# Optimization experiments

Measured on AMD Instinct MI355X. Metric: run time of the kernel, lower is better.

## Reference

```python
import jax, jax.numpy as jnp
import numpy as np

B, C, N, K, D = 4, 64, 40960, 16, 128
EPS = 1e-5  # BatchNorm2d default eps


def _bn_relu(x, g, b, m, v):
    # inference BN over channel axis 1, then ReLU (pt_utils.Conv2d default activation)
    scale = g / jnp.sqrt(v + EPS)
    shift = b - m * scale
    return jax.nn.relu(x * scale[None, :, None, None] + shift[None, :, None, None])


def setup_inputs() -> dict:
    key = jax.random.key(0)
    ks = jax.random.split(key, 16)
    feature = jax.random.normal(ks[0], (B, C, N, 1), jnp.float32)
    neigh_idx = jax.random.randint(ks[1], (B, N, K), 0, N)
    w1 = jax.random.normal(ks[2], (C, C), jnp.float32) * 0.05
    w2 = jax.random.normal(ks[3], (D, C), jnp.float32) * 0.05
    w3 = jax.random.normal(ks[4], (D, C), jnp.float32) * 0.05
    def bn(kg, km, kv, n):
        g = 1.0 + 0.1 * jax.random.normal(kg, (n,), jnp.float32)
        b = 0.1 * jax.random.normal(km, (n,), jnp.float32)
        m = 0.1 * jax.random.normal(kv, (n,), jnp.float32)
        v = jax.random.uniform(jax.random.fold_in(kv, 1), (n,), jnp.float32, 0.5, 1.5)
        return g, b, m, v
    g1, b1, m1, v1 = bn(ks[5], ks[6], ks[7], C)
    g2, b2, m2, v2 = bn(ks[8], ks[9], ks[10], D)
    g3, b3, m3, v3 = bn(ks[11], ks[12], ks[13], D)
    return dict(feature=feature, neigh_idx=neigh_idx,
                w1=w1, g1=g1, b1=b1, m1=m1, v1=v1,
                w2=w2, g2=g2, b2=b2, m2=m2, v2=v2,
                w3=w3, g3=g3, b3=b3, m3=m3, v3=v3)


def reference(feature, neigh_idx, w1, g1, b1, m1, v1, w2, g2, b2, m2, v2,
              w3, g3, b3, m3, v3):
    # gather_neighbour: feature [B,C,N,1], neigh_idx [B,N,K] -> [B,C,N,K]
    f = feature[:, :, :, 0]                                   # [B,C,N]
    f_neigh = jax.vmap(lambda fb, ib: fb[:, ib])(f, neigh_idx)  # [B,C,N,K]
    # mlp1: 1x1 conv + BN + ReLU
    h = jnp.einsum('oc,bcnk->bonk', w1, f_neigh)
    h = _bn_relu(h, g1, b1, m1, v1)
    # sum over neighbors
    h = jnp.sum(h, axis=-1, keepdims=True)                    # [B,C,N,1]
    # mlp2
    h = jnp.einsum('oc,bcnk->bonk', w2, h)
    h = _bn_relu(h, g2, b2, m2, v2)
    # mlp3 on original feature (residual branch)
    s = jnp.einsum('oc,bcnk->bonk', w3, feature)
    s = _bn_relu(s, g3, b3, m3, v3)
    return h + s                                              # [B,D,N,1]
```

## Files before the change

### kernel.cpp

```cpp
#include <hip/hip_runtime.h>

#define EPSV 1e-5f
constexpr int Bb = 4, Cc = 64, Nn = 40960, Kk = 16, Dd = 128;
constexpr int G = 4;
constexpr int TPB = Nn / 16;

typedef float f32x4 __attribute__((ext_vector_type(4)));
typedef __bf16 bf16x8 __attribute__((ext_vector_type(8)));
typedef unsigned short us8 __attribute__((ext_vector_type(8)));
typedef unsigned short us4 __attribute__((ext_vector_type(4)));

__device__ inline unsigned short f2bf(float x) {
    unsigned u = __builtin_bit_cast(unsigned, x);
    u += 0x7FFFu + ((u >> 16) & 1u);
    return (unsigned short)(u >> 16);
}

__global__ __launch_bounds__(256) void prep_weights(
    const float* __restrict__ w1, const float* __restrict__ g1, const float* __restrict__ b1,
    const float* __restrict__ m1, const float* __restrict__ v1,
    const float* __restrict__ w2, const float* __restrict__ g2, const float* __restrict__ b2,
    const float* __restrict__ m2, const float* __restrict__ v2,
    const float* __restrict__ w3, const float* __restrict__ g3, const float* __restrict__ b3,
    const float* __restrict__ m3, const float* __restrict__ v3,
    unsigned short* __restrict__ w1s, unsigned short* __restrict__ w2s, unsigned short* __restrict__ w3s,
    float* __restrict__ sh1, float* __restrict__ sh2, float* __restrict__ sh3) {
    const int e = blockIdx.x * 256 + threadIdx.x;
    if (e < 4096) {
        const int o = e >> 6;
        const float sc = g1[o] * rsqrtf(v1[o] + EPSV);
        w1s[e] = f2bf(w1[e] * sc);
    } else if (e < 12288) {
        const int i = e - 4096, o = i >> 6;
        const float sc = g2[o] * rsqrtf(v2[o] + EPSV);
        w2s[i] = f2bf(w2[i] * sc);
    } else if (e < 20480) {
        const int i = e - 12288, o = i >> 6;
        const float sc = g3[o] * rsqrtf(v3[o] + EPSV);
        w3s[i] = f2bf(w3[i] * sc);
    }
    if (e < 64) sh1[e] = b1[e] - m1[e] * (g1[e] * rsqrtf(v1[e] + EPSV));
    else if (e < 192) { const int d = e - 64;  sh2[d] = b2[d] - m2[d] * (g2[d] * rsqrtf(v2[d] + EPSV)); }
    else if (e < 320) { const int d = e - 192; sh3[d] = b3[d] - m3[d] * (g3[d] * rsqrtf(v3[d] + EPSV)); }
}

__global__ __launch_bounds__(256) void passA(const float* __restrict__ f,
                                             const unsigned short* __restrict__ w1s,
                                             const float* __restrict__ sh1,
                                             unsigned short* __restrict__ G1,
                                             unsigned short* __restrict__ f_t) {
    __shared__ float s[64 * 65];
    __shared__ __attribute__((aligned(16))) unsigned short sg1[64 * 72];

    const int tid = threadIdx.x, w = tid >> 6, lane = tid & 63;
    const int c15 = lane & 15, q = lane >> 4;
    const int b = blockIdx.x / 640;
    const int n0 = (blockIdx.x % 640) * 64;

    const float* src = f + ((size_t)b * Cc + w * 16) * Nn + n0 + lane;
#pragma unroll
    for (int i = 0; i < 16; ++i) s[(w * 16 + i) * 65 + lane] = src[(size_t)i * Nn];

    const int o1 = w * 16 + c15;
    const float sh1v = sh1[o1];
    bf16x8 bw1[2];
#pragma unroll
    for (int ks = 0; ks < 2; ++ks)
        bw1[ks] = __builtin_bit_cast(bf16x8, *(const uint4*)(w1s + o1 * 64 + ks * 32 + q * 8));
    __syncthreads();

#pragma unroll
    for (int mt = 0; mt < 4; ++mt) {
        const int pt = mt * 16 + c15;
        us8 A0, A1;
#pragma unroll
        for (int j = 0; j < 8; ++j) A0[j] = f2bf(s[(q * 8 + j) * 65 + pt]);
#pragma unroll
        for (int j = 0; j < 8; ++j) A1[j] = f2bf(s[(32 + q * 8 + j) * 65 + pt]);

        if (mt == w) {
            unsigned short* dst = f_t + ((size_t)b * Nn + n0 + pt) * 64;
            *(uint4*)(dst + q * 8)      = __builtin_bit_cast(uint4, A0);
            *(uint4*)(dst + 32 + q * 8) = __builtin_bit_cast(uint4, A1);
        }

        f32x4 g = {0.f, 0.f, 0.f, 0.f};
        g = __builtin_amdgcn_mfma_f32_16x16x32_bf16(__builtin_bit_cast(bf16x8, A0), bw1[0], g, 0, 0, 0);
        g = __builtin_amdgcn_mfma_f32_16x16x32_bf16(__builtin_bit_cast(bf16x8, A1), bw1[1], g, 0, 0, 0);
#pragma unroll
        for (int r = 0; r < 4; ++r)
            sg1[(mt * 16 + q * 4 + r) * 72 + o1] = f2bf(fmaxf(g[r] + sh1v, 0.f));
    }
    __syncthreads();

    {
        const int p = tid >> 2, ck = tid & 3;
        const uint4 v0 = *(const uint4*)(sg1 + p * 72 + ck * 16);
        const uint4 v1 = *(const uint4*)(sg1 + p * 72 + ck * 16 + 8);
        unsigned short* dst = G1 + ((size_t)b * Nn + n0 + p) * 64 + ck * 16;
        *(uint4*)dst = v0;
        *(uint4*)(dst + 8) = v1;
    }
}

__global__ __launch_bounds__(256, 4) void passB(
    const unsigned short* __restrict__ G1, const unsigned short* __restrict__ f_t,
    const int* __restrict__ idx,
    const unsigned short* __restrict__ w2s, const unsigned short* __restrict__ w3s,
    const float* __restrict__ sh2, const float* __restrict__ sh3,
    float* __restrict__ out) {
    __shared__ __attribute__((aligned(16))) unsigned short s_h1[16 * 72];
    __shared__ float s_out[32 * 133];

    const int tid  = threadIdx.x;
    const int wave = tid >> 6;
    const int lane = tid & 63;
    const int c15  = lane & 15;
    const int q    = lane >> 4;
    const int pg   = tid >> 4;
    const int cg   = tid & 15;

    const int xcd = blockIdx.x & 7;
    const int jb  = blockIdx.x >> 3;
    const int b   = xcd >> 1;
    const int nb0 = (((xcd & 1) * 320) + jb) * (G * 16);

    float sh2v[2], sh3v[2];
    bf16x8 bw2[2][2], bw3[2][2];
#pragma unroll
    for (int nt = 0; nt < 2; ++nt) {
        const int d = wave * 32 + nt * 16 + c15;
        sh2v[nt] = sh2[d];
        sh3v[nt] = sh3[d];
#pragma unroll
        for (int ks = 0; ks < 2; ++ks) {
            bw2[nt][ks] = __builtin_bit_cast(bf16x8, *(const uint4*)(w2s + d * 64 + ks * 32 + q * 8));
            bw3[nt][ks] = __builtin_bit_cast(bf16x8, *(const uint4*)(w3s + d * 64 + ks * 32 + q * 8));
        }
    }

    const unsigned short* G1b = G1 + (size_t)b * Nn * 64;
    const unsigned short* ftb = f_t + (size_t)b * Nn * 64;
    const int* idxp = idx + ((size_t)b * Nn + nb0) * Kk;

    int myidx = idxp[tid];

    for (int g = 0; g < G; ++g) {
        const int n0 = nb0 + g * 16;

        const int myidxN = (g + 1 < G) ? idxp[(g + 1) * 256 + tid] : 0;

        const unsigned short* ftrow = ftb + (size_t)(n0 + c15) * 64;
        const bf16x8 af0 = __builtin_bit_cast(bf16x8, *(const uint4*)(ftrow + q * 8));
        const bf16x8 af1 = __builtin_bit_cast(bf16x8, *(const uint4*)(ftrow + 32 + q * 8));

        float a0 = 0.f, a1 = 0.f, a2 = 0.f, a3 = 0.f;
#pragma unroll
        for (int k = 0; k < 16; ++k) {
            const int nb = __shfl(myidx, (pg & 3) * 16 + k, 64);
            const uint2 d2 = *(const uint2*)(G1b + (size_t)nb * 64 + cg * 4);
            a0 += __builtin_bit_cast(float, d2.x << 16);
            a1 += __builtin_bit_cast(float, d2.x & 0xffff0000u);
            a2 += __builtin_bit_cast(float, d2.y << 16);
            a3 += __builtin_bit_cast(float, d2.y & 0xffff0000u);
        }
        myidx = myidxN;

        __syncthreads();
        us4 hv;
        hv[0] = f2bf(a0); hv[1] = f2bf(a1); hv[2] = f2bf(a2); hv[3] = f2bf(a3);
        *(us4*)(s_h1 + pg * 72 + cg * 4) = hv;
        __syncthreads();

        const unsigned short* h1row = s_h1 + c15 * 72;
        const bf16x8 ah0 = __builtin_bit_cast(bf16x8, *(const uint4*)(h1row + q * 8));
        const bf16x8 ah1 = __builtin_bit_cast(bf16x8, *(const uint4*)(h1row + 32 + q * 8));

        const int prow = (g & 1) * 16;
#pragma unroll
        for (int nt = 0; nt < 2; ++nt) {
            f32x4 h2 = {sh2v[nt], sh2v[nt], sh2v[nt], sh2v[nt]};
            f32x4 s3 = {sh3v[nt], sh3v[nt], sh3v[nt], sh3v[nt]};
            h2 = __builtin_amdgcn_mfma_f32_16x16x32_bf16(ah0, bw2[nt][0], h2, 0, 0, 0);
            h2 = __builtin_amdgcn_mfma_f32_16x16x32_bf16(ah1, bw2[nt][1], h2, 0, 0, 0);
            s3 = __builtin_amdgcn_mfma_f32_16x16x32_bf16(af0, bw3[nt][0], s3, 0, 0, 0);
            s3 = __builtin_amdgcn_mfma_f32_16x16x32_bf16(af1, bw3[nt][1], s3, 0, 0, 0);
            const int d = wave * 32 + nt * 16 + c15;
#pragma unroll
            for (int r = 0; r < 4; ++r)
                s_out[(prow + q * 4 + r) * 133 + d] = fmaxf(h2[r], 0.f) + fmaxf(s3[r], 0.f);
        }
        __syncthreads();

        if (g & 1) {
            const int np = n0 - 16;
            const int dd = tid >> 3;
            const int ck = tid & 7;
#pragma unroll
            for (int r4 = 0; r4 < 4; ++r4) {
                const int d = r4 * 32 + dd;
                f32x4 v;
#pragma unroll
                for (int i = 0; i < 4; ++i) v[i] = s_out[(ck * 4 + i) * 133 + d];
                __builtin_nontemporal_store(v, (f32x4*)(out + ((size_t)b * Dd + d) * Nn + np + ck * 4));
            }
        }
    }
}

extern "C" void kernel_launch(void* const* d_in, const int* in_sizes, int n_in,
                              void* d_out, int out_size, void* d_ws, size_t ws_size,
                              hipStream_t stream) {
    const float* feature = (const float*)d_in[0];
    const int*   neigh   = (const int*)d_in[1];
    const float* w1 = (const float*)d_in[2];
    const float* g1 = (const float*)d_in[3];
    const float* b1 = (const float*)d_in[4];
    const float* m1 = (const float*)d_in[5];
    const float* v1 = (const float*)d_in[6];
    const float* w2 = (const float*)d_in[7];
    const float* g2 = (const float*)d_in[8];
    const float* b2 = (const float*)d_in[9];
    const float* m2 = (const float*)d_in[10];
    const float* v2 = (const float*)d_in[11];
    const float* w3 = (const float*)d_in[12];
    const float* g3 = (const float*)d_in[13];
    const float* b3 = (const float*)d_in[14];
    const float* m3 = (const float*)d_in[15];
    const float* v3 = (const float*)d_in[16];
    float* out = (float*)d_out;

    const size_t SZ_G1 = (size_t)Bb * Nn * 64 * 2;
    const size_t SZ_FT = (size_t)Bb * Nn * 64 * 2;

    char* ws = (char*)d_ws;
    unsigned short* G1  = (unsigned short*)ws;
    unsigned short* f_t = (unsigned short*)(ws + SZ_G1);
    char* wbase = ws + SZ_G1 + SZ_FT;

    unsigned short* w1s = (unsigned short*)wbase;
    unsigned short* w2s = (unsigned short*)(wbase + 8192);
    unsigned short* w3s = (unsigned short*)(wbase + 24576);
    float* sh1 = (float*)(wbase + 40960);
    float* sh2 = (float*)(wbase + 41216);
    float* sh3 = (float*)(wbase + 41728);

    prep_weights<<<80, 256, 0, stream>>>(w1, g1, b1, m1, v1, w2, g2, b2, m2, v2,
                                         w3, g3, b3, m3, v3, w1s, w2s, w3s, sh1, sh2, sh3);
    passA<<<Bb * 640, 256, 0, stream>>>(feature, w1s, sh1, G1, f_t);
    passB<<<(Bb * TPB) / G, 256, 0, stream>>>(G1, f_t, neigh, w2s, w3s,
                                              sh2, sh3, out);
}
```

Baseline: 209.9 us.

## Fuse weight prep, pass A and pass B into one cooperative persistent kernel

Replaces the three separate launches (weight prep, passA, passB) with one persistent cooperative kernel. Each block folds the BN scales into the weights itself, runs passA tiles in a grid-stride loop, waits at a grid-wide barrier, then runs passB groups with an XCD-aware remapping of work. The aim is to remove launch gaps and the kernel-boundary drain between passes. In exchange it adds a grid sync, redundant per-block weight preparation, and relies on the occupancy check allowing 1024 or more resident blocks.

```diff
diff --git a/kernel.cpp b/kernel.cpp
--- a/kernel.cpp
+++ b/kernel.cpp
@@ -1,9 +1,12 @@
 #include <hip/hip_runtime.h>
+#include <hip/hip_cooperative_groups.h>
 
 #define EPSV 1e-5f
 constexpr int Bb = 4, Cc = 64, Nn = 40960, Kk = 16, Dd = 128;
 constexpr int G = 4;
 constexpr int TPB = Nn / 16;
+constexpr int NTILE_A = Bb * 640;
+constexpr int NGRP_B  = (Bb * TPB) / G;
 
 typedef float f32x4 __attribute__((ext_vector_type(4)));
 typedef __bf16 bf16x8 __attribute__((ext_vector_type(8)));
@@ -14,6 +17,186 @@
     unsigned u = __builtin_bit_cast(unsigned, x);
     u += 0x7FFFu + ((u >> 16) & 1u);
     return (unsigned short)(u >> 16);
+}
+
+__global__ __launch_bounds__(256, 5) void fused(
+    const float* __restrict__ f, const int* __restrict__ idx,
+    const float* __restrict__ w1, const float* __restrict__ g1, const float* __restrict__ b1,
+    const float* __restrict__ m1, const float* __restrict__ v1,
+    const float* __restrict__ w2, const float* __restrict__ g2, const float* __restrict__ b2,
+    const float* __restrict__ m2, const float* __restrict__ v2,
+    const float* __restrict__ w3, const float* __restrict__ g3, const float* __restrict__ b3,
+    const float* __restrict__ m3, const float* __restrict__ v3,
+    unsigned short* __restrict__ G1, unsigned short* __restrict__ f_t,
+    float* __restrict__ out, const int nwg) {
+    __shared__ __attribute__((aligned(16))) char smem[25856];
+    float* s            = (float*)smem;
+    unsigned short* sg1 = (unsigned short*)(smem + 16640);
+    unsigned short* s_h1 = (unsigned short*)smem;
+    float* s_out        = (float*)(smem + 2304);
+
+    const int tid = threadIdx.x, wave = tid >> 6, lane = tid & 63;
+    const int c15 = lane & 15, q = lane >> 4;
+    const int bid = blockIdx.x;
+
+    {
+        const int o1 = wave * 16 + c15;
+        const float sc1 = g1[o1] * rsqrtf(v1[o1] + EPSV);
+        const float sh1v = b1[o1] - m1[o1] * sc1;
+        bf16x8 bw1[2];
+#pragma unroll
+        for (int ks = 0; ks < 2; ++ks) {
+            us8 t;
+#pragma unroll
+            for (int j = 0; j < 8; ++j) t[j] = f2bf(w1[o1 * 64 + ks * 32 + q * 8 + j] * sc1);
+            bw1[ks] = __builtin_bit_cast(bf16x8, t);
+        }
+
+        for (int tt = bid; tt < NTILE_A; tt += nwg) {
+            const int b = tt / 640;
+            const int n0 = (tt - b * 640) * 64;
+
+            const float* src = f + ((size_t)b * Cc + wave * 16) * Nn + n0 + lane;
+#pragma unroll
+            for (int i = 0; i < 16; ++i) s[(wave * 16 + i) * 65 + lane] = src[(size_t)i * Nn];
+            __syncthreads();
+
+#pragma unroll
+            for (int mt = 0; mt < 4; ++mt) {
+                const int pt = mt * 16 + c15;
+                us8 A0, A1;
+#pragma unroll
+                for (int j = 0; j < 8; ++j) A0[j] = f2bf(s[(q * 8 + j) * 65 + pt]);
+#pragma unroll
+                for (int j = 0; j < 8; ++j) A1[j] = f2bf(s[(32 + q * 8 + j) * 65 + pt]);
+
+                if (mt == wave) {
+                    unsigned short* dst = f_t + ((size_t)b * Nn + n0 + pt) * 64;
+                    *(uint4*)(dst + q * 8)      = __builtin_bit_cast(uint4, A0);
+                    *(uint4*)(dst + 32 + q * 8) = __builtin_bit_cast(uint4, A1);
+                }
+
+                f32x4 g = {0.f, 0.f, 0.f, 0.f};
+                g = __builtin_amdgcn_mfma_f32_16x16x32_bf16(__builtin_bit_cast(bf16x8, A0), bw1[0], g, 0, 0, 0);
+                g = __builtin_amdgcn_mfma_f32_16x16x32_bf16(__builtin_bit_cast(bf16x8, A1), bw1[1], g, 0, 0, 0);
+#pragma unroll
+                for (int r = 0; r < 4; ++r)
+                    sg1[(mt * 16 + q * 4 + r) * 72 + (wave * 16 + c15)] = f2bf(fmaxf(g[r] + sh1v, 0.f));
+            }
+            __syncthreads();
+
+            {
+                const int p = tid >> 2, ck = tid & 3;
+                const uint4 v0 = *(const uint4*)(sg1 + p * 72 + ck * 16);
+                const uint4 v1 = *(const uint4*)(sg1 + p * 72 + ck * 16 + 8);
+                unsigned short* dst = G1 + ((size_t)b * Nn + n0 + p) * 64 + ck * 16;
+                *(uint4*)dst = v0;
+                *(uint4*)(dst + 8) = v1;
+            }
+            __syncthreads();
+        }
+    }
+
+    float sh2v[2], sh3v[2];
+    bf16x8 bw2[2][2], bw3[2][2];
+#pragma unroll
+    for (int nt = 0; nt < 2; ++nt) {
+        const int d = wave * 32 + nt * 16 + c15;
+        const float sc2 = g2[d] * rsqrtf(v2[d] + EPSV);
+        const float sc3 = g3[d] * rsqrtf(v3[d] + EPSV);
+        sh2v[nt] = b2[d] - m2[d] * sc2;
+        sh3v[nt] = b3[d] - m3[d] * sc3;
+#pragma unroll
+        for (int ks = 0; ks < 2; ++ks) {
+            us8 t2, t3;
+#pragma unroll
+            for (int j = 0; j < 8; ++j) {
+                t2[j] = f2bf(w2[d * 64 + ks * 32 + q * 8 + j] * sc2);
+                t3[j] = f2bf(w3[d * 64 + ks * 32 + q * 8 + j] * sc3);
+            }
+            bw2[nt][ks] = __builtin_bit_cast(bf16x8, t2);
+            bw3[nt][ks] = __builtin_bit_cast(bf16x8, t3);
+        }
+    }
+
+    cooperative_groups::this_grid().sync();
+
+    const int pg = tid >> 4;
+    const int cg = tid & 15;
+
+    for (int v = bid; v < NGRP_B; v += nwg) {
+        const int xcd = v & 7;
+        const int jb  = v >> 3;
+        const int b   = xcd >> 1;
+        const int nb0 = (((xcd & 1) * 320) + jb) * (G * 16);
+
+        const unsigned short* G1b = G1 + (size_t)b * Nn * 64;
+        const unsigned short* ftb = f_t + (size_t)b * Nn * 64;
+        const int* idxp = idx + ((size_t)b * Nn + nb0) * Kk;
+
+        int myidx = idxp[tid];
+
+        for (int g = 0; g < G; ++g) {
+            const int n0 = nb0 + g * 16;
+            const int myidxN = (g + 1 < G) ? idxp[(g + 1) * 256 + tid] : 0;
+
+            const unsigned short* ftrow = ftb + (size_t)(n0 + c15) * 64;
+            const bf16x8 af0 = __builtin_bit_cast(bf16x8, *(const uint4*)(ftrow + q * 8));
+            const bf16x8 af1 = __builtin_bit_cast(bf16x8, *(const uint4*)(ftrow + 32 + q * 8));
+
+            float a0 = 0.f, a1 = 0.f, a2 = 0.f, a3 = 0.f;
+#pragma unroll
+            for (int k = 0; k < 16; ++k) {
+                const int nb = __shfl(myidx, (pg & 3) * 16 + k, 64);
+                const uint2 d2 = *(const uint2*)(G1b + (size_t)nb * 64 + cg * 4);
+                a0 += __builtin_bit_cast(float, d2.x << 16);
+                a1 += __builtin_bit_cast(float, d2.x & 0xffff0000u);
+                a2 += __builtin_bit_cast(float, d2.y << 16);
+                a3 += __builtin_bit_cast(float, d2.y & 0xffff0000u);
+            }
+            myidx = myidxN;
+
+            __syncthreads();
+            us4 hv;
+            hv[0] = f2bf(a0); hv[1] = f2bf(a1); hv[2] = f2bf(a2); hv[3] = f2bf(a3);
+            *(us4*)(s_h1 + pg * 72 + cg * 4) = hv;
+            __syncthreads();
+
+            const unsigned short* h1row = s_h1 + c15 * 72;
+            const bf16x8 ah0 = __builtin_bit_cast(bf16x8, *(const uint4*)(h1row + q * 8));
+            const bf16x8 ah1 = __builtin_bit_cast(bf16x8, *(const uint4*)(h1row + 32 + q * 8));
+
+            const int prow = (g & 1) * 16;
+#pragma unroll
+            for (int nt = 0; nt < 2; ++nt) {
+                f32x4 h2 = {sh2v[nt], sh2v[nt], sh2v[nt], sh2v[nt]};
+                f32x4 s3 = {sh3v[nt], sh3v[nt], sh3v[nt], sh3v[nt]};
+                h2 = __builtin_amdgcn_mfma_f32_16x16x32_bf16(ah0, bw2[nt][0], h2, 0, 0, 0);
+                h2 = __builtin_amdgcn_mfma_f32_16x16x32_bf16(ah1, bw2[nt][1], h2, 0, 0, 0);
+                s3 = __builtin_amdgcn_mfma_f32_16x16x32_bf16(af0, bw3[nt][0], s3, 0, 0, 0);
+                s3 = __builtin_amdgcn_mfma_f32_16x16x32_bf16(af1, bw3[nt][1], s3, 0, 0, 0);
+                const int d = wave * 32 + nt * 16 + c15;
+#pragma unroll
+                for (int r = 0; r < 4; ++r)
+                    s_out[(prow + q * 4 + r) * 133 + d] = fmaxf(h2[r], 0.f) + fmaxf(s3[r], 0.f);
+            }
+            __syncthreads();
+
+            if (g & 1) {
+                const int np = n0 - 16;
+                const int dd = tid >> 3;
+                const int ck = tid & 7;
+#pragma unroll
+                for (int r4 = 0; r4 < 4; ++r4) {
+                    const int d = r4 * 32 + dd;
+                    f32x4 vv;
+#pragma unroll
+                    for (int i = 0; i < 4; ++i) vv[i] = s_out[(ck * 4 + i) * 133 + d];
+                    __builtin_nontemporal_store(vv, (f32x4*)(out + ((size_t)b * Dd + d) * Nn + np + ck * 4));
+                }
+            }
+        }
+    }
 }
 
 __global__ __launch_bounds__(256) void prep_weights(
@@ -77,13 +260,11 @@
         for (int j = 0; j < 8; ++j) A0[j] = f2bf(s[(q * 8 + j) * 65 + pt]);
 #pragma unroll
         for (int j = 0; j < 8; ++j) A1[j] = f2bf(s[(32 + q * 8 + j) * 65 + pt]);
-
         if (mt == w) {
             unsigned short* dst = f_t + ((size_t)b * Nn + n0 + pt) * 64;
             *(uint4*)(dst + q * 8)      = __builtin_bit_cast(uint4, A0);
             *(uint4*)(dst + 32 + q * 8) = __builtin_bit_cast(uint4, A1);
         }
-
         f32x4 g = {0.f, 0.f, 0.f, 0.f};
         g = __builtin_amdgcn_mfma_f32_16x16x32_bf16(__builtin_bit_cast(bf16x8, A0), bw1[0], g, 0, 0, 0);
         g = __builtin_amdgcn_mfma_f32_16x16x32_bf16(__builtin_bit_cast(bf16x8, A1), bw1[1], g, 0, 0, 0);
@@ -147,7 +328,6 @@
 
     for (int g = 0; g < G; ++g) {
         const int n0 = nb0 + g * 16;
-
         const int myidxN = (g + 1 < G) ? idxp[(g + 1) * 256 + tid] : 0;
 
         const unsigned short* ftrow = ftb + (size_t)(n0 + c15) * 64;
@@ -238,16 +418,44 @@
     unsigned short* f_t = (unsigned short*)(ws + SZ_G1);
     char* wbase = ws + SZ_G1 + SZ_FT;
 
-    unsigned short* w1s = (unsigned short*)wbase;
-    unsigned short* w2s = (unsigned short*)(wbase + 8192);
-    unsigned short* w3s = (unsigned short*)(wbase + 24576);
-    float* sh1 = (float*)(wbase + 40960);
-    float* sh2 = (float*)(wbase + 41216);
-    float* sh3 = (float*)(wbase + 41728);
-
-    prep_weights<<<80, 256, 0, stream>>>(w1, g1, b1, m1, v1, w2, g2, b2, m2, v2,
-                                         w3, g3, b3, m3, v3, w1s, w2s, w3s, sh1, sh2, sh3);
-    passA<<<Bb * 640, 256, 0, stream>>>(feature, w1s, sh1, G1, f_t);
-    passB<<<(Bb * TPB) / G, 256, 0, stream>>>(G1, f_t, neigh, w2s, w3s,
-                                              sh2, sh3, out);
-}
+    static int coop_grid = []() -> int {
+        int dev = 0;
+        if (hipGetDevice(&dev) != hipSuccess) return 0;
+        int attr = 0;
+        if (hipDeviceGetAttribute(&attr, hipDeviceAttributeCooperativeLaunch, dev) != hipSuccess || !attr)
+            return 0;
+        int nb = 0;
+        if (hipOccupancyMaxActiveBlocksPerMultiprocessor(&nb, fused, 256, 0) != hipSuccess)
+            return 0;
+        int ncu = 0;
+        if (hipDeviceGetAttribute(&ncu, hipDeviceAttributeMultiprocessorCount, dev) != hipSuccess)
+            return 0;
+        const long cap = (long)nb * (long)ncu;
+        if (cap >= 1280) return 1280;
+        if (cap >= 1024) return 1024;
+        return 0;
+    }();
+
+    if (coop_grid > 0) {
+        int nwg = coop_grid;
+        void* args[] = {
+            (void*)&feature, (void*)&neigh,
+            (void*)&w1, (void*)&g1, (void*)&b1, (void*)&m1, (void*)&v1,
+            (void*)&w2, (void*)&g2, (void*)&b2, (void*)&m2, (void*)&v2,
+            (void*)&w3, (void*)&g3, (void*)&b3, (void*)&m3, (void*)&v3,
+            (void*)&G1, (void*)&f_t, (void*)&out, (void*)&nwg};
+        (void)hipLaunchCooperativeKernel((const void*)fused, dim3(nwg), dim3(256), args, 0, stream);
+    } else {
+        unsigned short* w1s = (unsigned short*)wbase;
+        unsigned short* w2s = (unsigned short*)(wbase + 8192);
+        unsigned short* w3s = (unsigned short*)(wbase + 24576);
+        float* sh1 = (float*)(wbase + 40960);
+        float* sh2 = (float*)(wbase + 41216);
+        float* sh3 = (float*)(wbase + 41728);
+        prep_weights<<<80, 256, 0, stream>>>(w1, g1, b1, m1, v1, w2, g2, b2, m2, v2,
+                                             w3, g3, b3, m3, v3, w1s, w2s, w3s, sh1, sh2, sh3);
+        passA<<<Bb * 640, 256, 0, stream>>>(feature, w1s, sh1, G1, f_t);
+        passB<<<(Bb * TPB) / G, 256, 0, stream>>>(G1, f_t, neigh, w2s, w3s,
+                                                  sh2, sh3, out);
+    }
+}
```

Result: no change. 210.3 us (+0.2%).

## Restructure passA to skip LDS staging and double-buffer passB h1 tile

Applied to the files above, without the earlier changes.

passA now has each lane load its own point's 64 channels straight from global memory and convert them to bf16 in registers. The float LDS transpose tile and one barrier go away, and the MFMA operands are swapped so the weights act as A and the features as B. passB double-buffers the s_h1 tile by group parity, which removes one barrier per group, and the s_out barrier now runs only on odd groups before the store. The risks are strided per-lane global loads in passA, which coalesce across lanes but read each channel row separately, and subtle races on s_out between even and odd groups.

```diff
diff --git a/kernel.cpp b/kernel.cpp
--- a/kernel.cpp
+++ b/kernel.cpp
@@ -49,55 +49,50 @@
                                              const float* __restrict__ sh1,
                                              unsigned short* __restrict__ G1,
                                              unsigned short* __restrict__ f_t) {
-    __shared__ float s[64 * 65];
     __shared__ __attribute__((aligned(16))) unsigned short sg1[64 * 72];
 
     const int tid = threadIdx.x, w = tid >> 6, lane = tid & 63;
     const int c15 = lane & 15, q = lane >> 4;
     const int b = blockIdx.x / 640;
     const int n0 = (blockIdx.x % 640) * 64;
-
-    const float* src = f + ((size_t)b * Cc + w * 16) * Nn + n0 + lane;
-#pragma unroll
-    for (int i = 0; i < 16; ++i) s[(w * 16 + i) * 65 + lane] = src[(size_t)i * Nn];
-
-    const int o1 = w * 16 + c15;
-    const float sh1v = sh1[o1];
-    bf16x8 bw1[2];
-#pragma unroll
-    for (int ks = 0; ks < 2; ++ks)
-        bw1[ks] = __builtin_bit_cast(bf16x8, *(const uint4*)(w1s + o1 * 64 + ks * 32 + q * 8));
+    const int p  = n0 + w * 16 + c15;
+
+    const float* fp = f + (size_t)b * Cc * Nn + p;
+    us8 F0, F1;
+#pragma unroll
+    for (int j = 0; j < 8; ++j) F0[j] = f2bf(fp[(size_t)(q * 8 + j) * Nn]);
+#pragma unroll
+    for (int j = 0; j < 8; ++j) F1[j] = f2bf(fp[(size_t)(32 + q * 8 + j) * Nn]);
+
+    {
+        unsigned short* dst = f_t + ((size_t)b * Nn + p) * 64 + q * 8;
+        *(uint4*)dst        = __builtin_bit_cast(uint4, F0);
+        *(uint4*)(dst + 32) = __builtin_bit_cast(uint4, F1);
+    }
+
+    const bf16x8 bf0 = __builtin_bit_cast(bf16x8, F0);
+    const bf16x8 bf1 = __builtin_bit_cast(bf16x8, F1);
+
+#pragma unroll
+    for (int nt = 0; nt < 4; ++nt) {
+        const int oa = nt * 16 + c15;
+        const bf16x8 aw0 = __builtin_bit_cast(bf16x8, *(const uint4*)(w1s + oa * 64 + q * 8));
+        const bf16x8 aw1 = __builtin_bit_cast(bf16x8, *(const uint4*)(w1s + oa * 64 + 32 + q * 8));
+        f32x4 acc = {0.f, 0.f, 0.f, 0.f};
+        acc = __builtin_amdgcn_mfma_f32_16x16x32_bf16(aw0, bf0, acc, 0, 0, 0);
+        acc = __builtin_amdgcn_mfma_f32_16x16x32_bf16(aw1, bf1, acc, 0, 0, 0);
+        const f32x4 shv = *(const f32x4*)(sh1 + nt * 16 + q * 4);
+#pragma unroll
+        for (int r = 0; r < 4; ++r)
+            sg1[(w * 16 + c15) * 72 + nt * 16 + q * 4 + r] = f2bf(fmaxf(acc[r] + shv[r], 0.f));
+    }
     __syncthreads();
 
-#pragma unroll
-    for (int mt = 0; mt < 4; ++mt) {
-        const int pt = mt * 16 + c15;
-        us8 A0, A1;
-#pragma unroll
-        for (int j = 0; j < 8; ++j) A0[j] = f2bf(s[(q * 8 + j) * 65 + pt]);
-#pragma unroll
-        for (int j = 0; j < 8; ++j) A1[j] = f2bf(s[(32 + q * 8 + j) * 65 + pt]);
-
-        if (mt == w) {
-            unsigned short* dst = f_t + ((size_t)b * Nn + n0 + pt) * 64;
-            *(uint4*)(dst + q * 8)      = __builtin_bit_cast(uint4, A0);
-            *(uint4*)(dst + 32 + q * 8) = __builtin_bit_cast(uint4, A1);
-        }
-
-        f32x4 g = {0.f, 0.f, 0.f, 0.f};
-        g = __builtin_amdgcn_mfma_f32_16x16x32_bf16(__builtin_bit_cast(bf16x8, A0), bw1[0], g, 0, 0, 0);
-        g = __builtin_amdgcn_mfma_f32_16x16x32_bf16(__builtin_bit_cast(bf16x8, A1), bw1[1], g, 0, 0, 0);
-#pragma unroll
-        for (int r = 0; r < 4; ++r)
-            sg1[(mt * 16 + q * 4 + r) * 72 + o1] = f2bf(fmaxf(g[r] + sh1v, 0.f));
-    }
-    __syncthreads();
-
     {
-        const int p = tid >> 2, ck = tid & 3;
-        const uint4 v0 = *(const uint4*)(sg1 + p * 72 + ck * 16);
-        const uint4 v1 = *(const uint4*)(sg1 + p * 72 + ck * 16 + 8);
-        unsigned short* dst = G1 + ((size_t)b * Nn + n0 + p) * 64 + ck * 16;
+        const int pt = tid >> 2, ck = tid & 3;
+        const uint4 v0 = *(const uint4*)(sg1 + pt * 72 + ck * 16);
+        const uint4 v1 = *(const uint4*)(sg1 + pt * 72 + ck * 16 + 8);
+        unsigned short* dst = G1 + ((size_t)b * Nn + n0 + pt) * 64 + ck * 16;
         *(uint4*)dst = v0;
         *(uint4*)(dst + 8) = v1;
     }
@@ -109,7 +104,7 @@
     const unsigned short* __restrict__ w2s, const unsigned short* __restrict__ w3s,
     const float* __restrict__ sh2, const float* __restrict__ sh3,
     float* __restrict__ out) {
-    __shared__ __attribute__((aligned(16))) unsigned short s_h1[16 * 72];
+    __shared__ __attribute__((aligned(16))) unsigned short s_h1[2][16 * 72];
     __shared__ float s_out[32 * 133];
 
     const int tid  = threadIdx.x;
@@ -166,13 +161,14 @@
         }
         myidx = myidxN;
 
+        {
+            us4 hv;
+            hv[0] = f2bf(a0); hv[1] = f2bf(a1); hv[2] = f2bf(a2); hv[3] = f2bf(a3);
+            *(us4*)(&s_h1[g & 1][0] + pg * 72 + cg * 4) = hv;
+        }
         __syncthreads();
-        us4 hv;
-        hv[0] = f2bf(a0); hv[1] = f2bf(a1); hv[2] = f2bf(a2); hv[3] = f2bf(a3);
-        *(us4*)(s_h1 + pg * 72 + cg * 4) = hv;
-        __syncthreads();
-
-        const unsigned short* h1row = s_h1 + c15 * 72;
+
+        const unsigned short* h1row = &s_h1[g & 1][0] + c15 * 72;
         const bf16x8 ah0 = __builtin_bit_cast(bf16x8, *(const uint4*)(h1row + q * 8));
         const bf16x8 ah1 = __builtin_bit_cast(bf16x8, *(const uint4*)(h1row + 32 + q * 8));
 
@@ -190,9 +186,9 @@
             for (int r = 0; r < 4; ++r)
                 s_out[(prow + q * 4 + r) * 133 + d] = fmaxf(h2[r], 0.f) + fmaxf(s3[r], 0.f);
         }
-        __syncthreads();
 
         if (g & 1) {
+            __syncthreads();
             const int np = n0 - 16;
             const int dd = tid >> 3;
             const int ck = tid & 7;
```

New measurement: 210.6 us. About the same (+0.3%).
